# Kernel optimization log

Hardware: AMD Instinct MI355X
Metric: run time of the kernel (lower is better)

Reference implementation:

```python
import jax, jax.numpy as jnp
import numpy as np

ROUTINGS = 3

def squash(x):
    # x: [..., O]; squash along last dim
    norm = jnp.linalg.norm(x, axis=-1, keepdims=True)
    scale = norm ** 2 / (1 + norm ** 2) / (norm + 1e-9)
    return scale * x

def setup_inputs() -> dict:
    key = jax.random.key(0)
    k1, k2 = jax.random.split(key)
    B, K, I, O, C = 256, 10, 1152, 16, 8
    x = jax.random.normal(k1, (B, I, C), dtype=jnp.float32)
    w = jax.random.normal(k2, (K, I, O, C), dtype=jnp.float32) * 0.05
    return {"x": x, "w": w}

def reference(x, w):
    # x: [B, I, Cin], w: [K, I, O, Cin]
    # u_hat[b,k,i,o] = sum_c w[k,i,o,c] * x[b,i,c]
    u_hat = jnp.einsum('kioc,bic->bkio', w, x)  # [B, K, I, O]
    B, K, I, O = u_hat.shape
    b = jnp.zeros((B, K, I, 1), dtype=u_hat.dtype)
    # routing iterations (fixed small loop); intermediate iters use detached u_hat
    u_hat_d = jax.lax.stop_gradient(u_hat)
    for _ in range(ROUTINGS - 1):
        c = jax.nn.softmax(b, axis=1)              # softmax over output capsules K
        s = jnp.sum(c * u_hat_d, axis=2)           # [B, K, O]
        v = squash(s)                              # [B, K, O]
        uv = jnp.einsum('bkio,bko->bki', u_hat_d, v)[..., None]  # [B, K, I, 1]
        b = b + uv
    c = jax.nn.softmax(b, axis=1)
    s = jnp.sum(c * u_hat, axis=2)
    v = squash(s)
    return v  # [B, K, O]
```

## Files before the change

kernel.cpp:

```cpp
#include <hip/hip_runtime.h>

#define B_ 256
#define K_ 10
#define I_ 1152
#define O_ 16
#define C_ 8

static __device__ __forceinline__ unsigned short f32_bf16(float f) {
    unsigned int u = __float_as_uint(f);
    u += 0x7FFFu + ((u >> 16) & 1u);
    return (unsigned short)(u >> 16);
}

__global__ __launch_bounds__(256) void uhat_kernel(
    const float* __restrict__ x, const float* __restrict__ w,
    unsigned short* __restrict__ u)
{
    __shared__ float w_lds[16 * 132];
    const int t   = threadIdx.x;
    const int i_l = t & 15, tg = t >> 4;
    const int i0  = blockIdx.x * 16;
    const int b0  = blockIdx.y * 64 + tg * 4;
    const int kb  = blockIdx.z * 2;
    const int i   = i0 + i_l;

    float4 xr[4][2];
#pragma unroll
    for (int bb = 0; bb < 4; bb++) {
        const float4* xp = (const float4*)(x + ((size_t)(b0 + bb) * I_ + i) * C_);
        xr[bb][0] = xp[0];
        xr[bb][1] = xp[1];
    }

#pragma unroll
    for (int kk = 0; kk < 2; kk++) {
        const int k = kb + kk;
        __syncthreads();
        const float4* ws = (const float4*)(w + ((size_t)k * I_ + i0) * O_ * C_);
#pragma unroll
        for (int r = 0; r < 2; r++) {
            int idx = r * 256 + t;
            int ii = idx >> 5, rem = idx & 31;
            *(float4*)&w_lds[ii * 132 + rem * 4] = ws[idx];
        }
        __syncthreads();

#pragma unroll
        for (int half = 0; half < 2; half++) {
            unsigned int pk[4][4];
#pragma unroll
            for (int oq = 0; oq < 4; oq++) {
                const int oo = half * 4 + oq;
                float d[4][2];
#pragma unroll
                for (int h = 0; h < 2; h++) {
                    const int o = oo * 2 + h;
                    const float4 w0 = *(const float4*)&w_lds[i_l * 132 + o * 8];
                    const float4 w1 = *(const float4*)&w_lds[i_l * 132 + o * 8 + 4];
#pragma unroll
                    for (int bb = 0; bb < 4; bb++) {
                        d[bb][h] = w0.x*xr[bb][0].x + w0.y*xr[bb][0].y
                                 + w0.z*xr[bb][0].z + w0.w*xr[bb][0].w
                                 + w1.x*xr[bb][1].x + w1.y*xr[bb][1].y
                                 + w1.z*xr[bb][1].z + w1.w*xr[bb][1].w;
                    }
                }
#pragma unroll
                for (int bb = 0; bb < 4; bb++)
                    pk[bb][oq] = (unsigned int)f32_bf16(d[bb][0]) |
                                 ((unsigned int)f32_bf16(d[bb][1]) << 16);
            }
#pragma unroll
            for (int bb = 0; bb < 4; bb++) {
                unsigned int* dst = (unsigned int*)
                    (u + (((size_t)(b0 + bb) * K_ + k) * I_ + i) * O_) + half * 4;
                *(uint4*)dst = make_uint4(pk[bb][0], pk[bb][1], pk[bb][2], pk[bb][3]);
            }
        }
    }
}

template <bool UNIFORM>
static __device__ __forceinline__ void sweep(
    const unsigned short* __restrict__ ub, int i_l,
    const float* __restrict__ v_lds, int og, float acc[K_][2])
{
#pragma unroll
    for (int k = 0; k < K_; k++) { acc[k][0] = 0.f; acc[k][1] = 0.f; }

    unsigned int P[K_], Q[K_];
#pragma unroll
    for (int k = 0; k < K_; k++)
        P[k] = *(const unsigned int*)(ub + ((size_t)k * I_ + i_l) * O_);

#pragma unroll 1
    for (int ic = 0; ic < 9; ic++) {
        if (ic + 1 < 9) {
            const int i = (ic + 1) * 128 + i_l;
#pragma unroll
            for (int k = 0; k < K_; k++)
                Q[k] = *(const unsigned int*)(ub + ((size_t)k * I_ + i) * O_);
        }
        float c[K_];
        if (!UNIFORM) {
            float Z = 0.f;
#pragma unroll
            for (int k = 0; k < K_; k++) {
                const float f0 = __uint_as_float(P[k] << 16);
                const float f1 = __uint_as_float(P[k] & 0xffff0000u);
                float lk = f0 * v_lds[k * 16 + og * 2]
                         + f1 * v_lds[k * 16 + og * 2 + 1];
                lk += __shfl_xor(lk, 1);
                lk += __shfl_xor(lk, 2);
                lk += __shfl_xor(lk, 4);
                c[k] = __expf(lk);
                Z += c[k];
            }
            const float inv = 1.0f / Z;
#pragma unroll
            for (int k = 0; k < K_; k++) c[k] *= inv;
        } else {
#pragma unroll
            for (int k = 0; k < K_; k++) c[k] = 1.0f;
        }
#pragma unroll
        for (int k = 0; k < K_; k++) {
            const float f0 = __uint_as_float(P[k] << 16);
            const float f1 = __uint_as_float(P[k] & 0xffff0000u);
            acc[k][0] = fmaf(c[k], f0, acc[k][0]);
            acc[k][1] = fmaf(c[k], f1, acc[k][1]);
        }
#pragma unroll
        for (int k = 0; k < K_; k++) P[k] = Q[k];
    }
}

static __device__ __forceinline__ void block_reduce(
    float acc[K_][2], float* __restrict__ red, int lane, int wv)
{
#pragma unroll
    for (int k = 0; k < K_; k++)
#pragma unroll
        for (int j = 0; j < 2; j++) {
            float a = acc[k][j];
            a += __shfl_xor(a, 8); a += __shfl_xor(a, 16); a += __shfl_xor(a, 32);
            acc[k][j] = a;
        }
    if (lane < 8) {
#pragma unroll
        for (int k = 0; k < K_; k++)
            *(float2*)&red[wv * 160 + k * 16 + lane * 2] =
                make_float2(acc[k][0], acc[k][1]);
    }
    __syncthreads();
}

static __device__ __forceinline__ float sum16(const float* __restrict__ red, int t)
{
    float s = 0.f;
#pragma unroll
    for (int wgi = 0; wgi < 16; wgi++) s += red[wgi * 160 + t];
    return s;
}

static __device__ __forceinline__ float squash_v(float s) {
    float n2 = s * s;
    n2 += __shfl_xor(n2, 1); n2 += __shfl_xor(n2, 2);
    n2 += __shfl_xor(n2, 4); n2 += __shfl_xor(n2, 8);
    const float norm = sqrtf(n2);
    return s * (n2 / (1.0f + n2) / (norm + 1e-9f));
}

__global__ __launch_bounds__(1024) void route_all(
    const unsigned short* __restrict__ u, float* __restrict__ out)
{
    __shared__ float red[16 * 160];
    __shared__ float v_lds[160];
    __shared__ float v1_lds[160];

    const int t    = threadIdx.x;
    const int og   = t & 7, i_l = t >> 3;
    const int b    = blockIdx.x;
    const int lane = t & 63, wv = t >> 6;

    const unsigned short* ub = u + (size_t)b * K_ * I_ * O_ + og * 2;
    float acc[K_][2];

    sweep<true>(ub, i_l, nullptr, og, acc);
    block_reduce(acc, red, lane, wv);
    if (t < 160) {
        float v = squash_v(sum16(red, t) * (1.0f / K_));
        v1_lds[t] = v;
        v_lds[t]  = v;
    }
    __syncthreads();

    sweep<false>(ub, i_l, v_lds, og, acc);
    block_reduce(acc, red, lane, wv);
    float v12 = 0.f;
    if (t < 160) v12 = v1_lds[t] + squash_v(sum16(red, t));
    __syncthreads();
    if (t < 160) v_lds[t] = v12;
    __syncthreads();

    sweep<false>(ub, i_l, v_lds, og, acc);
    block_reduce(acc, red, lane, wv);
    if (t < 160)
        out[(size_t)b * 160 + t] = squash_v(sum16(red, t));
}

extern "C" void kernel_launch(void* const* d_in, const int* in_sizes, int n_in,
                              void* d_out, int out_size, void* d_ws, size_t ws_size,
                              hipStream_t stream)
{
    const float* x = (const float*)d_in[0];
    const float* w = (const float*)d_in[1];
    float* outp = (float*)d_out;

    unsigned short* u = (unsigned short*)d_ws;

    uhat_kernel<<<dim3(72, 4, 5), 256, 0, stream>>>(x, w, u);
    route_all<<<B_, 1024, 0, stream>>>(u, outp);
}
```

Baseline: 140.2 us.

## Fuse first routing sum into u_hat kernel via DPP reductions and atomics

The first routing pass (uniform coefficients) is now computed inside the u_hat producer: each 16-lane row sums its d values with DPP adds and the row leader atomically adds the partial into an s1 buffer, which is zeroed by a memset beforehand. The routing kernel reads s1 directly and skips one full sweep over u_hat, cutting that pass's global reads. In exchange it adds a memset launch, many float atomics (72 partials per element), and non-deterministic summation order. It also sums in fp32 before bf16 rounding.

```diff
diff --git a/kernel.cpp b/kernel.cpp
--- a/kernel.cpp
+++ b/kernel.cpp
@@ -5,6 +5,7 @@
 #define I_ 1152
 #define O_ 16
 #define C_ 8
+#define BKO (B_*K_*O_)
 
 static __device__ __forceinline__ unsigned short f32_bf16(float f) {
     unsigned int u = __float_as_uint(f);
@@ -12,9 +13,22 @@
     return (unsigned short)(u >> 16);
 }
 
+template <int CTRL>
+static __device__ __forceinline__ float dpp_add(float v) {
+    int x = __builtin_amdgcn_update_dpp(0, __float_as_int(v), CTRL, 0xF, 0xF, true);
+    return v + __int_as_float(x);
+}
+static __device__ __forceinline__ float row16_sum(float v) {
+    v = dpp_add<0xB1>(v);
+    v = dpp_add<0x4E>(v);
+    v = dpp_add<0x141>(v);
+    v = dpp_add<0x140>(v);
+    return v;
+}
+
 __global__ __launch_bounds__(256) void uhat_kernel(
     const float* __restrict__ x, const float* __restrict__ w,
-    unsigned short* __restrict__ u)
+    unsigned short* __restrict__ u, float* __restrict__ s1)
 {
     __shared__ float w_lds[16 * 132];
     const int t   = threadIdx.x;
@@ -23,6 +37,7 @@
     const int b0  = blockIdx.y * 64 + tg * 4;
     const int kb  = blockIdx.z * 2;
     const int i   = i0 + i_l;
+    const bool row_leader = (i_l == 0);
 
     float4 xr[4][2];
 #pragma unroll
@@ -66,6 +81,16 @@
                     }
                 }
 #pragma unroll
+                for (int bb = 0; bb < 4; bb++) {
+#pragma unroll
+                    for (int h = 0; h < 2; h++) {
+                        const float rs = row16_sum(d[bb][h]);
+                        if (row_leader)
+                            atomicAdd(&s1[((size_t)(b0 + bb) * K_ + k) * O_
+                                          + oo * 2 + h], rs);
+                    }
+                }
+#pragma unroll
                 for (int bb = 0; bb < 4; bb++)
                     pk[bb][oq] = (unsigned int)f32_bf16(d[bb][0]) |
                                  ((unsigned int)f32_bf16(d[bb][1]) << 16);
@@ -80,7 +105,6 @@
     }
 }
 
-template <bool UNIFORM>
 static __device__ __forceinline__ void sweep(
     const unsigned short* __restrict__ ub, int i_l,
     const float* __restrict__ v_lds, int og, float acc[K_][2])
@@ -102,33 +126,27 @@
                 Q[k] = *(const unsigned int*)(ub + ((size_t)k * I_ + i) * O_);
         }
         float c[K_];
-        if (!UNIFORM) {
-            float Z = 0.f;
-#pragma unroll
-            for (int k = 0; k < K_; k++) {
-                const float f0 = __uint_as_float(P[k] << 16);
-                const float f1 = __uint_as_float(P[k] & 0xffff0000u);
-                float lk = f0 * v_lds[k * 16 + og * 2]
-                         + f1 * v_lds[k * 16 + og * 2 + 1];
-                lk += __shfl_xor(lk, 1);
-                lk += __shfl_xor(lk, 2);
-                lk += __shfl_xor(lk, 4);
-                c[k] = __expf(lk);
-                Z += c[k];
-            }
-            const float inv = 1.0f / Z;
-#pragma unroll
-            for (int k = 0; k < K_; k++) c[k] *= inv;
-        } else {
-#pragma unroll
-            for (int k = 0; k < K_; k++) c[k] = 1.0f;
-        }
+        float Z = 0.f;
 #pragma unroll
         for (int k = 0; k < K_; k++) {
             const float f0 = __uint_as_float(P[k] << 16);
             const float f1 = __uint_as_float(P[k] & 0xffff0000u);
-            acc[k][0] = fmaf(c[k], f0, acc[k][0]);
-            acc[k][1] = fmaf(c[k], f1, acc[k][1]);
+            float lk = f0 * v_lds[k * 16 + og * 2]
+                     + f1 * v_lds[k * 16 + og * 2 + 1];
+            lk += __shfl_xor(lk, 1);
+            lk += __shfl_xor(lk, 2);
+            lk += __shfl_xor(lk, 4);
+            c[k] = __expf(lk);
+            Z += c[k];
+        }
+        const float inv = 1.0f / Z;
+#pragma unroll
+        for (int k = 0; k < K_; k++) {
+            const float ck = c[k] * inv;
+            const float f0 = __uint_as_float(P[k] << 16);
+            const float f1 = __uint_as_float(P[k] & 0xffff0000u);
+            acc[k][0] = fmaf(ck, f0, acc[k][0]);
+            acc[k][1] = fmaf(ck, f1, acc[k][1]);
         }
 #pragma unroll
         for (int k = 0; k < K_; k++) P[k] = Q[k];
@@ -172,7 +190,8 @@
 }
 
 __global__ __launch_bounds__(1024) void route_all(
-    const unsigned short* __restrict__ u, float* __restrict__ out)
+    const unsigned short* __restrict__ u, const float* __restrict__ s1,
+    float* __restrict__ out)
 {
     __shared__ float red[16 * 160];
     __shared__ float v_lds[160];
@@ -186,16 +205,14 @@
     const unsigned short* ub = u + (size_t)b * K_ * I_ * O_ + og * 2;
     float acc[K_][2];
 
-    sweep<true>(ub, i_l, nullptr, og, acc);
-    block_reduce(acc, red, lane, wv);
     if (t < 160) {
-        float v = squash_v(sum16(red, t) * (1.0f / K_));
+        float v = squash_v(s1[(size_t)b * 160 + t] * (1.0f / K_));
         v1_lds[t] = v;
         v_lds[t]  = v;
     }
     __syncthreads();
 
-    sweep<false>(ub, i_l, v_lds, og, acc);
+    sweep(ub, i_l, v_lds, og, acc);
     block_reduce(acc, red, lane, wv);
     float v12 = 0.f;
     if (t < 160) v12 = v1_lds[t] + squash_v(sum16(red, t));
@@ -203,7 +220,7 @@
     if (t < 160) v_lds[t] = v12;
     __syncthreads();
 
-    sweep<false>(ub, i_l, v_lds, og, acc);
+    sweep(ub, i_l, v_lds, og, acc);
     block_reduce(acc, red, lane, wv);
     if (t < 160)
         out[(size_t)b * 160 + t] = squash_v(sum16(red, t));
@@ -217,8 +234,10 @@
     const float* w = (const float*)d_in[1];
     float* outp = (float*)d_out;
 
-    unsigned short* u = (unsigned short*)d_ws;
-
-    uhat_kernel<<<dim3(72, 4, 5), 256, 0, stream>>>(x, w, u);
-    route_all<<<B_, 1024, 0, stream>>>(u, outp);
-}
+    float* s1 = (float*)d_ws;
+    unsigned short* u = (unsigned short*)(s1 + BKO);
+
+    (void)hipMemsetAsync(s1, 0, (size_t)BKO * sizeof(float), stream);
+    uhat_kernel<<<dim3(72, 4, 5), 256, 0, stream>>>(x, w, u, s1);
+    route_all<<<B_, 1024, 0, stream>>>(u, s1, outp);
+}
```

Measured after the change: 311.5 us. 2.22x slower.
